# Kernel tuning notes

Measured on AMD Instinct MI355X. Metric: run time of the kernel, lower is better.

## Reference

```python
import jax, jax.numpy as jnp
import numpy as np

EPS = 1e-3  # BatchNorm eps from partial(nn.BatchNorm1d, eps=0.001)


def _bn(x, g, b, m, v):
    # inference-mode BatchNorm1d with running stats
    return (x - m) * jax.lax.rsqrt(v + EPS) * g + b


def setup_inputs() -> dict:
    key = jax.random.key(0)
    ks = jax.random.split(key, 24)
    N_REF, N_Q, E = 50_000, 50_000, 1_600_000
    C_IN, C0, C1 = 16, 32, 32
    s = 0.1
    return {
        "ref_bxyz": jax.random.normal(ks[0], (N_REF, 4), jnp.float32),
        "ref_feat": jax.random.normal(ks[1], (N_REF, C_IN), jnp.float32),
        "query_bxyz": jax.random.normal(ks[2], (N_Q, 4), jnp.float32),
        "e_ref": jax.random.randint(ks[3], (E,), 0, N_REF, jnp.int32),
        "e_query": jax.random.randint(ks[4], (E,), 0, N_Q, jnp.int32),
        "w_pos": jax.random.normal(ks[5], (3, C0), jnp.float32) * s,
        "bn0_g": jax.random.uniform(ks[6], (C0,), jnp.float32, 0.5, 1.5),
        "bn0_b": jax.random.normal(ks[7], (C0,), jnp.float32) * s,
        "bn0_m": jax.random.normal(ks[8], (C0,), jnp.float32) * s,
        "bn0_v": jax.random.uniform(ks[9], (C0,), jnp.float32, 0.5, 1.5),
        "w_feat": jax.random.normal(ks[10], (C_IN, C0), jnp.float32) * s,
        "bnf_g": jax.random.uniform(ks[11], (C0,), jnp.float32, 0.5, 1.5),
        "bnf_b": jax.random.normal(ks[12], (C0,), jnp.float32) * s,
        "bnf_m": jax.random.normal(ks[13], (C0,), jnp.float32) * s,
        "bnf_v": jax.random.uniform(ks[14], (C0,), jnp.float32, 0.5, 1.5),
        "w1": jax.random.normal(ks[15], (C0, C1), jnp.float32) * s,
        "b1": jax.random.normal(ks[16], (C1,), jnp.float32) * s,
        "bn1_g": jax.random.uniform(ks[17], (C1,), jnp.float32, 0.5, 1.5),
        "bn1_b": jax.random.normal(ks[18], (C1,), jnp.float32) * s,
        "bn1_m": jax.random.normal(ks[19], (C1,), jnp.float32) * s,
        "bn1_v": jax.random.uniform(ks[20], (C1,), jnp.float32, 0.5, 1.5),
    }


def reference(ref_bxyz, ref_feat, query_bxyz, e_ref, e_query,
              w_pos, bn0_g, bn0_b, bn0_m, bn0_v,
              w_feat, bnf_g, bnf_b, bnf_m, bnf_v,
              w1, b1, bn1_g, bn1_b, bn1_m, bn1_v):
    # gather: per-edge xyz difference (drop batch column 0)
    pos_diff = (ref_bxyz[e_ref] - query_bxyz[e_query])[:, 1:4]        # [E, 3]
    pos_feat = _bn(pos_diff @ w_pos, bn0_g, bn0_b, bn0_m, bn0_v)       # [E, C0]
    # node-level feature projection, then gather per edge
    ref_feat2 = _bn(ref_feat @ w_feat, bnf_g, bnf_b, bnf_m, bnf_v)     # [N_ref, C0]
    edge_feat = jax.nn.relu(pos_feat + ref_feat2[e_ref])               # [E, C0]
    # mlp_convs chain (single layer here: C0 -> C1 with bias)
    edge_feat = jax.nn.relu(_bn(edge_feat @ w1 + b1, bn1_g, bn1_b, bn1_m, bn1_v))  # [E, C1]
    # scatter-max aggregate into query nodes; empty segments -> 0 (torch_scatter semantics)
    n_q = query_bxyz.shape[0]
    q = jax.ops.segment_max(edge_feat, e_query, num_segments=n_q)      # [N_q, C1]
    return jnp.where(jnp.isfinite(q), q, jnp.zeros((), q.dtype))
```

## Files before the change

### kernel.cpp

```cpp
#include <hip/hip_runtime.h>

#define EPS 1e-3f
#define SYS 17
#define FRAG_OFF 1184
#define PK_OFF 1696
#define NSUP 32
#define SUPSLOTS 69632
#define BINB 512
#define WCAP 80
#define WRITERS 16

using frag_ab = __attribute__((ext_vector_type(8))) short;
using frag_cd = __attribute__((ext_vector_type(4))) float;

__device__ __forceinline__ unsigned pack_bf16_rne(float a, float b) {
    unsigned ua = __float_as_uint(a), ub = __float_as_uint(b);
    ua += 0x7FFFu + ((ua >> 16) & 1u);
    ub += 0x7FFFu + ((ub >> 16) & 1u);
    return (ua >> 16) | (ub & 0xFFFF0000u);
}
__device__ __forceinline__ float ubf_lo(unsigned u) { return __uint_as_float(u << 16); }
__device__ __forceinline__ float ubf_hi(unsigned u) { return __uint_as_float(u & 0xFFFF0000u); }

__global__ __launch_bounds__(256)
void mega_pre(const float* __restrict__ w_pos,
              const float* __restrict__ g0, const float* __restrict__ b0,
              const float* __restrict__ m0, const float* __restrict__ v0,
              const float* __restrict__ w1, const float* __restrict__ b1lin,
              const float* __restrict__ g1, const float* __restrict__ b1bn,
              const float* __restrict__ m1, const float* __restrict__ v1,
              const float* __restrict__ feat, const float* __restrict__ wf,
              const float* __restrict__ gf, const float* __restrict__ bf,
              const float* __restrict__ mf, const float* __restrict__ vf,
              const float4* __restrict__ bxyz,
              const int* __restrict__ e_query, const int* __restrict__ e_ref,
              float* __restrict__ ws, unsigned* __restrict__ ref2pk,
              uint2* __restrict__ pos_pk, int* __restrict__ supCur,
              unsigned* __restrict__ pairs1,
              int E, int n_ref, int nodeB, int posB) {
    __shared__ unsigned bkt[4 * NSUP * WCAP];
    __shared__ int cnt[4 * NSUP];
    __shared__ int gb[NSUP], woff[4 * NSUP];

    int b = blockIdx.x, t = threadIdx.x;

    if (b == 0) {
        if (t < 32) {
            int c = t;
            float s0 = g0[c] * rsqrtf(v0[c] + EPS);
            #pragma unroll
            for (int k = 0; k < 3; ++k) ws[k * 32 + c] = w_pos[k * 32 + c] * s0;
            ws[96 + c] = b0[c] - m0[c] * s0;
            float s1 = g1[c] * rsqrtf(v1[c] + EPS);
            #pragma unroll
            for (int k = 0; k < 32; ++k) ws[128 + k * 32 + c] = w1[k * 32 + c] * s1;
            ws[1152 + c] = (b1lin[c] - m1[c]) * s1 + b1bn[c];
        }
        __syncthreads();
        if (t < 64) {
            unsigned* wB = (unsigned*)ws + FRAG_OFF;
            int n = t & 15, quad = t >> 4;
            #pragma unroll
            for (int h = 0; h < 2; ++h) {
                int col = n + 16 * h;
                #pragma unroll
                for (int jp = 0; jp < 4; ++jp) {
                    int k = quad * 8 + 2 * jp;
                    wB[h * 256 + t * 4 + jp] =
                        pack_bf16_rne(ws[128 + k * 32 + col], ws[128 + (k + 1) * 32 + col]);
                }
            }
        }
        return;
    }
    b -= 1;
    if (b < nodeB) {
        int idx = b * 256 + t;
        if (idx < n_ref * 16) {
            int n = idx >> 4, cp = idx & 15;
            int c0 = 2 * cp, c1 = 2 * cp + 1;
            float a0 = 0.f, a1 = 0.f;
            #pragma unroll
            for (int k = 0; k < 16; ++k) {
                float fk = feat[n * 16 + k];
                a0 = fmaf(fk, wf[k * 32 + c0], a0);
                a1 = fmaf(fk, wf[k * 32 + c1], a1);
            }
            float s0 = gf[c0] * rsqrtf(vf[c0] + EPS);
            float s1 = gf[c1] * rsqrtf(vf[c1] + EPS);
            ref2pk[idx] = pack_bf16_rne((a0 - mf[c0]) * s0 + bf[c0],
                                        (a1 - mf[c1]) * s1 + bf[c1]);
        }
        return;
    }
    b -= nodeB;
    if (b < posB) {
        int i = b * 256 + t;
        if (i < n_ref) {
            float4 rb = bxyz[i];
            pos_pk[i] = make_uint2(pack_bf16_rne(rb.y, rb.z), pack_bf16_rne(rb.w, 0.f));
        }
        return;
    }
    b -= posB;
    int wv = t >> 6, lane = t & 63;
    if (t < 4 * NSUP) cnt[t] = 0;
    __syncthreads();
    int per = (E + BINB * 4 - 1) / (BINB * 4);
    int gid = b * 4 + wv;
    int e0 = gid * per, e1 = min(e0 + per, E);
    for (int e = e0 + lane; e < e1; e += 64) {
        int q = __builtin_nontemporal_load(e_query + e);
        int r = __builtin_nontemporal_load(e_ref + e);
        int s = q >> 11;
        int pos = atomicAdd(&cnt[wv * NSUP + s], 1);
        if (pos < WCAP) bkt[wv * (NSUP * WCAP) + s * WCAP + pos] =
            ((unsigned)(q & 2047) << 16) | (unsigned)r;
    }
    __syncthreads();
    if (t < NSUP) {
        int s = t;
        int n0 = min(cnt[s], WCAP),            n1 = min(cnt[NSUP + s], WCAP);
        int n2 = min(cnt[2 * NSUP + s], WCAP), n3 = min(cnt[3 * NSUP + s], WCAP);
        woff[s] = 0; woff[NSUP + s] = n0;
        woff[2 * NSUP + s] = n0 + n1; woff[3 * NSUP + s] = n0 + n1 + n2;
        gb[s] = (n0 + n1 + n2 + n3) ? atomicAdd(&supCur[s], n0 + n1 + n2 + n3) : 0;
    }
    __syncthreads();
    for (int s = 0; s < NSUP; ++s) {
        int n = min(cnt[wv * NSUP + s], WCAP);
        if (lane < n) {
            int g = gb[s] + woff[wv * NSUP + s] + lane;
            if (g < SUPSLOTS)
                pairs1[(size_t)s * SUPSLOTS + g] = bkt[wv * (NSUP * WCAP) + s * WCAP + lane];
        }
    }
}

__global__ __launch_bounds__(256)
void hist_kernel(const int* __restrict__ supCur, const unsigned* __restrict__ pairs1,
                 int* __restrict__ PH) {
    __shared__ int h[64];
    int s = blockIdx.x / WRITERS, w = blockIdx.x % WRITERS, t = threadIdx.x;
    if (t < 64) h[t] = 0;
    __syncthreads();
    int n = min(supCur[s], SUPSLOTS);
    int lo = (n * w) / WRITERS, hi = (n * (w + 1)) / WRITERS;
    const unsigned* base = pairs1 + (size_t)s * SUPSLOTS;
    for (int i = lo + t; i < hi; i += 256)
        atomicAdd(&h[(base[i] >> 21) & 63], 1);
    __syncthreads();
    if (t < 64) PH[(s * WRITERS + w) * 64 + t] = h[t];
}

__global__ __launch_bounds__(256)
void scan_kernel(const int* __restrict__ PH, int* __restrict__ finoffs,
                 int* __restrict__ WB) {
    __shared__ int ft[2048];
    __shared__ int part[256];
    int t = threadIdx.x;
    for (int fg = t; fg < 2048; fg += 256) {
        int s = fg >> 6, f = fg & 63, sum = 0;
        #pragma unroll
        for (int w = 0; w < WRITERS; ++w) sum += PH[(s * WRITERS + w) * 64 + f];
        ft[fg] = sum;
    }
    __syncthreads();
    int loc[8]; int run = 0;
    #pragma unroll
    for (int i = 0; i < 8; ++i) { loc[i] = run; run += ft[t * 8 + i]; }
    part[t] = run;
    __syncthreads();
    for (int d = 1; d < 256; d <<= 1) {
        int x = (t >= d) ? part[t - d] : 0;
        __syncthreads();
        part[t] += x;
        __syncthreads();
    }
    int total = part[255];
    int basep = part[t] - run;
    #pragma unroll
    for (int i = 0; i < 8; ++i) ft[t * 8 + i] = basep + loc[i];
    __syncthreads();
    for (int fg = t; fg < 2048; fg += 256) {
        int s = fg >> 6, f = fg & 63;
        int acc = ft[fg];
        #pragma unroll
        for (int w = 0; w < WRITERS; ++w) {
            WB[(s * WRITERS + w) * 64 + f] = acc;
            acc += PH[(s * WRITERS + w) * 64 + f];
        }
        finoffs[fg] = ft[fg];
    }
    if (t == 0) finoffs[2048] = total;
}

__global__ __launch_bounds__(256)
void scatter_kernel(const int* __restrict__ supCur, const unsigned* __restrict__ pairs1,
                    const int* __restrict__ WB, unsigned* __restrict__ pairs2) {
    __shared__ int basef[64], lcnt[64];
    int s = blockIdx.x / WRITERS, w = blockIdx.x % WRITERS, t = threadIdx.x;
    if (t < 64) { basef[t] = WB[(s * WRITERS + w) * 64 + t]; lcnt[t] = 0; }
    __syncthreads();
    int n = min(supCur[s], SUPSLOTS);
    int lo = (n * w) / WRITERS, hi = (n * (w + 1)) / WRITERS;
    const unsigned* src = pairs1 + (size_t)s * SUPSLOTS;
    for (int i = lo + t; i < hi; i += 256) {
        unsigned u = src[i];
        int f = (u >> 21) & 63;
        int pos = basef[f] + atomicAdd(&lcnt[f], 1);
        pairs2[pos] = u & 0x001FFFFFu;
    }
}

__global__ __launch_bounds__(256)
void fused_kernel(const uint2* __restrict__ pos_pk, const float4* __restrict__ query_bxyz,
                  const int* __restrict__ finoffs, const unsigned* __restrict__ pairs2,
                  const float* __restrict__ ws, float* __restrict__ out, int n_q) {
    __shared__ int outacc[32 * 33];
    __shared__ float4 qx[32];

    int t = threadIdx.x;
    int ln = t & 63, wv = t >> 6;
    int b = blockIdx.x;
    int q0 = b * 32;

    int start = finoffs[b], end = finoffs[b + 1];
    int w = end - start;
    if (t < 32) {
        int qq = q0 + t;
        qx[t] = query_bxyz[qq < n_q ? qq : 0];
    }
    for (int i = t; i < 32 * 33; i += 256) outacc[i] = 0;

    int mrow = ln & 15, cpg = ln >> 4;
    const float4* wsf4 = (const float4*)ws;
    float4 w0xa = wsf4[cpg * 2],          w0xb = wsf4[cpg * 2 + 1];
    float4 w0ya = wsf4[8 + cpg * 2],      w0yb = wsf4[8 + cpg * 2 + 1];
    float4 w0za = wsf4[16 + cpg * 2],     w0zb = wsf4[16 + cpg * 2 + 1];
    float4 b0a  = wsf4[24 + cpg * 2],     b0b  = wsf4[24 + cpg * 2 + 1];
    const int4* wB4 = (const int4*)((const unsigned*)ws + FRAG_OFF);
    frag_ab bfr0 = __builtin_bit_cast(frag_ab, wB4[ln]);
    frag_ab bfr1 = __builtin_bit_cast(frag_ab, wB4[64 + ln]);
    int ncol = ln & 15, quad = ln >> 4;
    float b1a = ws[1152 + ncol];
    float b1b = ws[1168 + ncol];
    const uint4* __restrict__ ref2pk = (const uint4*)((const unsigned*)ws + PK_OFF);
    __syncthreads();

    int nrt = (w + 15) >> 4;
    for (int rt = wv; rt < nrt; rt += 4) {
        int sg = rt * 16 + mrow;
        int lq = 0;
        unsigned pk0 = 0, pk1 = 0, pk2 = 0, pk3 = 0;
        if (sg < w) {
            unsigned u = __builtin_nontemporal_load(pairs2 + start + sg);
            lq = u >> 16;
            int r = u & 0xFFFFu;
            uint2 pp = pos_pk[r];
            float4 qb = qx[lq];
            float d0 = ubf_lo(pp.x) - qb.y;
            float d1 = ubf_hi(pp.x) - qb.z;
            float d2 = ubf_lo(pp.y) - qb.w;
            uint4 rf = ref2pk[r * 4 + cpg];
            float h0 = fmaxf(fmaf(d0, w0xa.x, fmaf(d1, w0ya.x, fmaf(d2, w0za.x, b0a.x))) + ubf_lo(rf.x), 0.f);
            float h1 = fmaxf(fmaf(d0, w0xa.y, fmaf(d1, w0ya.y, fmaf(d2, w0za.y, b0a.y))) + ubf_hi(rf.x), 0.f);
            float h2 = fmaxf(fmaf(d0, w0xa.z, fmaf(d1, w0ya.z, fmaf(d2, w0za.z, b0a.z))) + ubf_lo(rf.y), 0.f);
            float h3 = fmaxf(fmaf(d0, w0xa.w, fmaf(d1, w0ya.w, fmaf(d2, w0za.w, b0a.w))) + ubf_hi(rf.y), 0.f);
            float h4 = fmaxf(fmaf(d0, w0xb.x, fmaf(d1, w0yb.x, fmaf(d2, w0zb.x, b0b.x))) + ubf_lo(rf.z), 0.f);
            float h5 = fmaxf(fmaf(d0, w0xb.y, fmaf(d1, w0yb.y, fmaf(d2, w0zb.y, b0b.y))) + ubf_hi(rf.z), 0.f);
            float h6 = fmaxf(fmaf(d0, w0xb.z, fmaf(d1, w0yb.z, fmaf(d2, w0zb.z, b0b.z))) + ubf_lo(rf.w), 0.f);
            float h7 = fmaxf(fmaf(d0, w0xb.w, fmaf(d1, w0yb.w, fmaf(d2, w0zb.w, b0b.w))) + ubf_hi(rf.w), 0.f);
            pk0 = pack_bf16_rne(h0, h1);
            pk1 = pack_bf16_rne(h2, h3);
            pk2 = pack_bf16_rne(h4, h5);
            pk3 = pack_bf16_rne(h6, h7);
        }
        int4 ai = make_int4((int)pk0, (int)pk1, (int)pk2, (int)pk3);
        frag_ab af = __builtin_bit_cast(frag_ab, ai);
        frag_cd c0 = {b1a, b1a, b1a, b1a};
        frag_cd c1 = {b1b, b1b, b1b, b1b};
        c0 = __builtin_amdgcn_mfma_f32_16x16x32_bf16(af, bfr0, c0, 0, 0, 0);
        c1 = __builtin_amdgcn_mfma_f32_16x16x32_bf16(af, bfr1, c1, 0, 0, 0);
        int baserow = rt * 16 + quad * 4;
        #pragma unroll
        for (int rg = 0; rg < 4; ++rg) {
            int lqr = __shfl(lq, quad * 4 + rg, 64);
            if (baserow + rg < w) {
                atomicMax(&outacc[ncol * 33 + lqr],
                          __float_as_int(fmaxf(c0[rg], 0.f)));
                atomicMax(&outacc[(ncol + 16) * 33 + lqr],
                          __float_as_int(fmaxf(c1[rg], 0.f)));
            }
        }
    }
    __syncthreads();
    #pragma unroll
    for (int g = 0; g < 4; ++g) {
        int o = t + 256 * g;
        int qq = o >> 5, ch = o & 31;
        int qo = q0 + qq;
        if (qo < n_q)
            __builtin_nontemporal_store(__int_as_float(outacc[ch * 33 + qq]),
                                        out + (size_t)qo * 32 + ch);
    }
}

extern "C" void kernel_launch(void* const* d_in, const int* in_sizes, int n_in,
                              void* d_out, int out_size, void* d_ws, size_t ws_size,
                              hipStream_t stream) {
    const float* ref_bxyz   = (const float*)d_in[0];
    const float* ref_feat   = (const float*)d_in[1];
    const float* query_bxyz = (const float*)d_in[2];
    const int*   e_ref      = (const int*)d_in[3];
    const int*   e_query    = (const int*)d_in[4];
    const float* w_pos      = (const float*)d_in[5];
    const float* bn0_g = (const float*)d_in[6];
    const float* bn0_b = (const float*)d_in[7];
    const float* bn0_m = (const float*)d_in[8];
    const float* bn0_v = (const float*)d_in[9];
    const float* w_feat = (const float*)d_in[10];
    const float* bnf_g = (const float*)d_in[11];
    const float* bnf_b = (const float*)d_in[12];
    const float* bnf_m = (const float*)d_in[13];
    const float* bnf_v = (const float*)d_in[14];
    const float* w1    = (const float*)d_in[15];
    const float* b1    = (const float*)d_in[16];
    const float* bn1_g = (const float*)d_in[17];
    const float* bn1_b = (const float*)d_in[18];
    const float* bn1_m = (const float*)d_in[19];
    const float* bn1_v = (const float*)d_in[20];

    int n_ref = in_sizes[0] / 4;
    int n_q   = in_sizes[2] / 4;
    int E     = in_sizes[3];
    int nb    = (n_q + 31) >> 5;

    float* ws = (float*)d_ws;
    unsigned* base_u = (unsigned*)d_ws;
    size_t off = PK_OFF;
    unsigned* ref2pk = base_u + off;           off += (size_t)n_ref * 16;
    uint2*    pos_pk = (uint2*)(base_u + off); off += (size_t)n_ref * 2;
    int*      supCur = (int*)(base_u + off);   off += NSUP;
    int*      PH     = (int*)(base_u + off);   off += NSUP * WRITERS * 64;
    int*      WB     = (int*)(base_u + off);   off += NSUP * WRITERS * 64;
    int*      finoffs= (int*)(base_u + off);   off += 2049;
    off = (off + 63) & ~(size_t)63;
    unsigned* pairs1 = base_u + off;           off += (size_t)NSUP * SUPSLOTS;
    unsigned* pairs2 = base_u + off;           off += (size_t)E;

    int nodeB = (n_ref * 16 + 255) / 256;
    int posB  = (n_ref + 255) / 256;

    hipMemsetAsync(supCur, 0, NSUP * sizeof(int), stream);

    int megaGrid = 1 + nodeB + posB + BINB;
    mega_pre<<<megaGrid, 256, 0, stream>>>(
        w_pos, bn0_g, bn0_b, bn0_m, bn0_v, w1, b1, bn1_g, bn1_b, bn1_m, bn1_v,
        ref_feat, w_feat, bnf_g, bnf_b, bnf_m, bnf_v,
        (const float4*)ref_bxyz, e_query, e_ref,
        ws, ref2pk, pos_pk, supCur, pairs1, E, n_ref, nodeB, posB);

    hist_kernel<<<NSUP * WRITERS, 256, 0, stream>>>(supCur, pairs1, PH);
    scan_kernel<<<1, 256, 0, stream>>>(PH, finoffs, WB);
    scatter_kernel<<<NSUP * WRITERS, 256, 0, stream>>>(supCur, pairs1, WB, pairs2);

    fused_kernel<<<nb, 256, 0, stream>>>(
        pos_pk, (const float4*)query_bxyz,
        finoffs, pairs2, ws, (float*)d_out, n_q);
}
```

Before: 194.0 us.

## Software-pipeline edge gathers, use hardware bf16 pack, drop redundant relu, retune bins

The main edge loop now prefetches the next tile's pair index and its dependent gathers (pos, ref features, query coords) one iteration ahead, with the pair index loaded two ahead, so gather latency overlaps with the MFMA and atomic work. The software RNE bf16 pack is replaced with the v_cvt_pk_bf16_f32 instruction. The relu before the atomicMax is removed, relying on the zero-initialised accumulator and integer-ordered max of float bits to clamp negatives. BINB and WRITERS are doubled and the bucket flush loop strides by 64, which adds register pressure and changes the binning work split.

```diff
diff --git a/kernel.cpp b/kernel.cpp
--- a/kernel.cpp
+++ b/kernel.cpp
@@ -1,14 +1,13 @@
 #include <hip/hip_runtime.h>
 
 #define EPS 1e-3f
-#define SYS 17
 #define FRAG_OFF 1184
 #define PK_OFF 1696
 #define NSUP 32
 #define SUPSLOTS 69632
-#define BINB 512
+#define BINB 1024
 #define WCAP 80
-#define WRITERS 16
+#define WRITERS 32
 
 using frag_ab = __attribute__((ext_vector_type(8))) short;
 using frag_cd = __attribute__((ext_vector_type(4))) float;
@@ -18,6 +17,11 @@
     ua += 0x7FFFu + ((ua >> 16) & 1u);
     ub += 0x7FFFu + ((ub >> 16) & 1u);
     return (ua >> 16) | (ub & 0xFFFF0000u);
+}
+__device__ __forceinline__ unsigned cvt_pk_bf16(float a, float b) {
+    unsigned r;
+    asm("v_cvt_pk_bf16_f32 %0, %1, %2" : "=v"(r) : "v"(a), "v"(b));
+    return r;
 }
 __device__ __forceinline__ float ubf_lo(unsigned u) { return __uint_as_float(u << 16); }
 __device__ __forceinline__ float ubf_hi(unsigned u) { return __uint_as_float(u & 0xFFFF0000u); }
@@ -129,10 +133,10 @@
     __syncthreads();
     for (int s = 0; s < NSUP; ++s) {
         int n = min(cnt[wv * NSUP + s], WCAP);
-        if (lane < n) {
-            int g = gb[s] + woff[wv * NSUP + s] + lane;
+        for (int l = lane; l < n; l += 64) {
+            int g = gb[s] + woff[wv * NSUP + s] + l;
             if (g < SUPSLOTS)
-                pairs1[(size_t)s * SUPSLOTS + g] = bkt[wv * (NSUP * WCAP) + s * WCAP + lane];
+                pairs1[(size_t)s * SUPSLOTS + g] = bkt[wv * (NSUP * WCAP) + s * WCAP + l];
         }
     }
 }
@@ -249,34 +253,50 @@
     __syncthreads();
 
     int nrt = (w + 15) >> 4;
+
+    auto ldu = [&](int rt) -> unsigned {
+        if (rt >= nrt) return 0u;
+        int sg = rt * 16 + mrow;
+        int idx = sg < w ? sg : (w - 1);
+        return __builtin_nontemporal_load(pairs2 + start + idx);
+    };
+
+    unsigned u_c = 0;
+    uint2 pp_c = {}; uint4 rf_c = {}; float4 qb_c = {};
+    if (wv < nrt) {
+        u_c = ldu(wv);
+        int r = u_c & 0xFFFFu;
+        pp_c = pos_pk[r];
+        rf_c = ref2pk[r * 4 + cpg];
+        qb_c = qx[u_c >> 16];
+    }
+    unsigned u_n = ldu(wv + 4);
+
     for (int rt = wv; rt < nrt; rt += 4) {
-        int sg = rt * 16 + mrow;
-        int lq = 0;
-        unsigned pk0 = 0, pk1 = 0, pk2 = 0, pk3 = 0;
-        if (sg < w) {
-            unsigned u = __builtin_nontemporal_load(pairs2 + start + sg);
-            lq = u >> 16;
-            int r = u & 0xFFFFu;
-            uint2 pp = pos_pk[r];
-            float4 qb = qx[lq];
-            float d0 = ubf_lo(pp.x) - qb.y;
-            float d1 = ubf_hi(pp.x) - qb.z;
-            float d2 = ubf_lo(pp.y) - qb.w;
-            uint4 rf = ref2pk[r * 4 + cpg];
-            float h0 = fmaxf(fmaf(d0, w0xa.x, fmaf(d1, w0ya.x, fmaf(d2, w0za.x, b0a.x))) + ubf_lo(rf.x), 0.f);
-            float h1 = fmaxf(fmaf(d0, w0xa.y, fmaf(d1, w0ya.y, fmaf(d2, w0za.y, b0a.y))) + ubf_hi(rf.x), 0.f);
-            float h2 = fmaxf(fmaf(d0, w0xa.z, fmaf(d1, w0ya.z, fmaf(d2, w0za.z, b0a.z))) + ubf_lo(rf.y), 0.f);
-            float h3 = fmaxf(fmaf(d0, w0xa.w, fmaf(d1, w0ya.w, fmaf(d2, w0za.w, b0a.w))) + ubf_hi(rf.y), 0.f);
-            float h4 = fmaxf(fmaf(d0, w0xb.x, fmaf(d1, w0yb.x, fmaf(d2, w0zb.x, b0b.x))) + ubf_lo(rf.z), 0.f);
-            float h5 = fmaxf(fmaf(d0, w0xb.y, fmaf(d1, w0yb.y, fmaf(d2, w0zb.y, b0b.y))) + ubf_hi(rf.z), 0.f);
-            float h6 = fmaxf(fmaf(d0, w0xb.z, fmaf(d1, w0yb.z, fmaf(d2, w0zb.z, b0b.z))) + ubf_lo(rf.w), 0.f);
-            float h7 = fmaxf(fmaf(d0, w0xb.w, fmaf(d1, w0yb.w, fmaf(d2, w0zb.w, b0b.w))) + ubf_hi(rf.w), 0.f);
-            pk0 = pack_bf16_rne(h0, h1);
-            pk1 = pack_bf16_rne(h2, h3);
-            pk2 = pack_bf16_rne(h4, h5);
-            pk3 = pack_bf16_rne(h6, h7);
-        }
-        int4 ai = make_int4((int)pk0, (int)pk1, (int)pk2, (int)pk3);
+        int rtn = rt + 4;
+        uint2 pp_n = {}; uint4 rf_n = {}; float4 qb_n = {};
+        if (rtn < nrt) {
+            int rn = u_n & 0xFFFFu;
+            pp_n = pos_pk[rn];
+            rf_n = ref2pk[rn * 4 + cpg];
+            qb_n = qx[u_n >> 16];
+        }
+        unsigned u_n2 = ldu(rtn + 4);
+
+        int lq = u_c >> 16;
+        float d0 = ubf_lo(pp_c.x) - qb_c.y;
+        float d1 = ubf_hi(pp_c.x) - qb_c.z;
+        float d2 = ubf_lo(pp_c.y) - qb_c.w;
+        float h0 = fmaxf(fmaf(d0, w0xa.x, fmaf(d1, w0ya.x, fmaf(d2, w0za.x, b0a.x))) + ubf_lo(rf_c.x), 0.f);
+        float h1 = fmaxf(fmaf(d0, w0xa.y, fmaf(d1, w0ya.y, fmaf(d2, w0za.y, b0a.y))) + ubf_hi(rf_c.x), 0.f);
+        float h2 = fmaxf(fmaf(d0, w0xa.z, fmaf(d1, w0ya.z, fmaf(d2, w0za.z, b0a.z))) + ubf_lo(rf_c.y), 0.f);
+        float h3 = fmaxf(fmaf(d0, w0xa.w, fmaf(d1, w0ya.w, fmaf(d2, w0za.w, b0a.w))) + ubf_hi(rf_c.y), 0.f);
+        float h4 = fmaxf(fmaf(d0, w0xb.x, fmaf(d1, w0yb.x, fmaf(d2, w0zb.x, b0b.x))) + ubf_lo(rf_c.z), 0.f);
+        float h5 = fmaxf(fmaf(d0, w0xb.y, fmaf(d1, w0yb.y, fmaf(d2, w0zb.y, b0b.y))) + ubf_hi(rf_c.z), 0.f);
+        float h6 = fmaxf(fmaf(d0, w0xb.z, fmaf(d1, w0yb.z, fmaf(d2, w0zb.z, b0b.z))) + ubf_lo(rf_c.w), 0.f);
+        float h7 = fmaxf(fmaf(d0, w0xb.w, fmaf(d1, w0yb.w, fmaf(d2, w0zb.w, b0b.w))) + ubf_hi(rf_c.w), 0.f);
+        int4 ai = make_int4((int)cvt_pk_bf16(h0, h1), (int)cvt_pk_bf16(h2, h3),
+                            (int)cvt_pk_bf16(h4, h5), (int)cvt_pk_bf16(h6, h7));
         frag_ab af = __builtin_bit_cast(frag_ab, ai);
         frag_cd c0 = {b1a, b1a, b1a, b1a};
         frag_cd c1 = {b1b, b1b, b1b, b1b};
@@ -287,12 +307,12 @@
         for (int rg = 0; rg < 4; ++rg) {
             int lqr = __shfl(lq, quad * 4 + rg, 64);
             if (baserow + rg < w) {
-                atomicMax(&outacc[ncol * 33 + lqr],
-                          __float_as_int(fmaxf(c0[rg], 0.f)));
-                atomicMax(&outacc[(ncol + 16) * 33 + lqr],
-                          __float_as_int(fmaxf(c1[rg], 0.f)));
+                atomicMax(&outacc[ncol * 33 + lqr], __float_as_int(c0[rg]));
+                atomicMax(&outacc[(ncol + 16) * 33 + lqr], __float_as_int(c1[rg]));
             }
         }
+        u_c = u_n; pp_c = pp_n; rf_c = rf_n; qb_c = qb_n;
+        u_n = u_n2;
     }
     __syncthreads();
     #pragma unroll
```

Result: no change. 195.6 us (+0.8%).
